# Kernel optimization log

Measured on AMD Instinct MI355X. Metric: run time of the kernel, lower is better.

Reference implementation:

```python
import jax, jax.numpy as jnp
import numpy as np

B, CIN, C, H, W = 4, 256, 128, 64, 64
LN_EPS = 1e-5


def _conv1x1(x, Wk, bk):
    # x: [B, Cin, H, W], Wk: [Cout, Cin] -> [B, Cout, H, W]
    return jnp.einsum('bchw,oc->bohw', x, Wk) + bk[None, :, None, None]


def setup_inputs() -> dict:
    key = jax.random.key(0)
    ks = jax.random.split(key, 11)
    s_in = 1.0 / np.sqrt(CIN)
    s_c = 1.0 / np.sqrt(C)
    return {
        'x': jax.random.normal(ks[0], (B, CIN, H, W), jnp.float32),
        'Wg': jax.random.normal(ks[1], (C, CIN), jnp.float32) * s_in,
        'bg': jax.random.normal(ks[2], (C,), jnp.float32) * s_in,
        'Wt': jax.random.normal(ks[3], (C, CIN), jnp.float32) * s_in,
        'bt': jax.random.normal(ks[4], (C,), jnp.float32) * s_in,
        'Wp': jax.random.normal(ks[5], (C, CIN), jnp.float32) * s_in,
        'bp': jax.random.normal(ks[6], (C,), jnp.float32) * s_in,
        'Wz': jax.random.normal(ks[7], (CIN, C), jnp.float32) * s_c,
        'bz': jax.random.normal(ks[8], (CIN,), jnp.float32) * s_c,
        'gamma': jax.random.normal(ks[9], (CIN, H, W), jnp.float32),
        'beta': jax.random.normal(ks[10], (CIN,), jnp.float32).reshape(CIN, 1, 1) * jnp.ones((CIN, H, W), jnp.float32),
    }


def reference(x, Wg, bg, Wt, bt, Wp, bp, Wz, bz, gamma, beta):
    b, cin, h, w = x.shape
    n = h * w
    # 1x1 conv projections -> flatten spatial
    g = _conv1x1(x, Wg, bg).reshape(b, C, n).transpose(0, 2, 1)      # [B, N, C]
    theta = _conv1x1(x, Wt, bt).reshape(b, C, n).transpose(0, 2, 1)  # [B, N, C]
    phi = _conv1x1(x, Wp, bp).reshape(b, C, n)                        # [B, C, N]
    # embedded-gaussian attention: no scaling, softmax over keys
    f = jnp.einsum('bnc,bcm->bnm', theta, phi)                        # [B, N, N]
    attn = jax.nn.softmax(f, axis=-1)
    y = jnp.einsum('bnm,bmc->bnc', attn, g)                           # [B, N, C]
    y = y.transpose(0, 2, 1).reshape(b, C, h, w)                      # [B, C, H, W]
    # output projection + LayerNorm over [Cin, H, W]
    z = _conv1x1(y, Wz, bz)                                           # [B, Cin, H, W]
    mean = jnp.mean(z, axis=(1, 2, 3), keepdims=True)
    var = jnp.var(z, axis=(1, 2, 3), keepdims=True)
    ln = (z - mean) * jax.lax.rsqrt(var + LN_EPS) * gamma[None] + beta[None]
    return ln + x
```

## Files before the change

kernel.cpp:

```cpp
#include <hip/hip_runtime.h>
#include <hip/hip_bf16.h>


#define BB   4
#define CINC 256
#define CCH  128
#define NS   4096
#define LN_EPS 1e-5f

typedef unsigned short ushort_t;
typedef unsigned int   uint_t;
typedef __bf16 bf16x8 __attribute__((ext_vector_type(8)));
typedef float  f32x4  __attribute__((ext_vector_type(4)));
typedef float  f32x16 __attribute__((ext_vector_type(16)));

typedef const __attribute__((address_space(1))) void* gas_ptr;
typedef __attribute__((address_space(3))) void*       las_ptr;

__device__ __forceinline__ void gload16(const ushort_t* g, ushort_t* l) {
    __builtin_amdgcn_global_load_lds((gas_ptr)g, (las_ptr)l, 16, 0, 0);
}

__device__ __forceinline__ float4 ld4(const float* p) { return *reinterpret_cast<const float4*>(p); }
__device__ __forceinline__ void   st4(float* p, float4 v) { *reinterpret_cast<float4*>(p) = v; }

__device__ __forceinline__ ushort_t f2bf(float f) {
    __hip_bfloat16 h = __float2bfloat16(f);
    return *reinterpret_cast<ushort_t*>(&h);
}
__device__ __forceinline__ float bf2f(ushort_t u) {
    __hip_bfloat16 h = *reinterpret_cast<__hip_bfloat16*>(&u);
    return __bfloat162float(h);
}
__device__ __forceinline__ uint_t pk2(float a, float b) {
    return (uint_t)f2bf(a) | ((uint_t)f2bf(b) << 16);
}

__device__ __forceinline__ float dot4(float4 a, float4 b) {
    return a.x * b.x + a.y * b.y + a.z * b.z + a.w * b.w;
}

__global__ __launch_bounds__(256) void split_kernel(
    const float* __restrict__ x,
    ushort_t* __restrict__ xTh, ushort_t* __restrict__ xTl)
{
    __shared__ float T[64 * 68];

    const int tid = threadIdx.x;
    const int n0  = blockIdx.x * 64;
    const int k0  = blockIdx.y * 64;
    const int b   = blockIdx.z;

#pragma unroll
    for (int u = 0; u < 4; ++u) {
        int fi = u * 256 + tid;
        int k  = fi >> 4;
        int c4 = fi & 15;
        float4 v = ld4(&x[(size_t)(b * CINC + k0 + k) * NS + n0 + c4 * 4]);
        T[(c4 * 4 + 0) * 68 + k] = v.x;
        T[(c4 * 4 + 1) * 68 + k] = v.y;
        T[(c4 * 4 + 2) * 68 + k] = v.z;
        T[(c4 * 4 + 3) * 68 + k] = v.w;
    }
    __syncthreads();

#pragma unroll
    for (int u = 0; u < 2; ++u) {
        int fi = u * 256 + tid;
        int n  = fi >> 3;
        int j  = fi & 7;
        float4 a0 = ld4(&T[n * 68 + j * 8]);
        float4 a1 = ld4(&T[n * 68 + j * 8 + 4]);
        float v[8] = {a0.x, a0.y, a0.z, a0.w, a1.x, a1.y, a1.z, a1.w};
        uint_t hw[4], lw[4];
#pragma unroll
        for (int jj = 0; jj < 4; ++jj) {
            ushort_t h0 = f2bf(v[2 * jj]);
            ushort_t h1 = f2bf(v[2 * jj + 1]);
            ushort_t e0 = f2bf(v[2 * jj] - bf2f(h0));
            ushort_t e1 = f2bf(v[2 * jj + 1] - bf2f(h1));
            hw[jj] = (uint_t)h0 | ((uint_t)h1 << 16);
            lw[jj] = (uint_t)e0 | ((uint_t)e1 << 16);
        }
        size_t base = (size_t)(b * NS + n0 + n) * CINC + k0 + ((j ^ (n & 7)) * 8);
        *reinterpret_cast<uint4*>(&xTh[base]) = make_uint4(hw[0], hw[1], hw[2], hw[3]);
        *reinterpret_cast<uint4*>(&xTl[base]) = make_uint4(lw[0], lw[1], lw[2], lw[3]);
    }
}

__global__ __launch_bounds__(256) void wsplit_kernel(
    const float* __restrict__ Wt, const float* __restrict__ Wp,
    const float* __restrict__ Wg,
    ushort_t* __restrict__ Whs, ushort_t* __restrict__ Wls)
{
    int task = blockIdx.x * 256 + threadIdx.x;
    if (task >= 384 * 32) return;
    int o = task >> 5;
    int j = task & 31;
    int mid = o >> 7;
    int r   = o & 127;
    const float* Wsel = (mid == 0) ? Wt : (mid == 1) ? Wp : Wg;
    float4 a0 = ld4(&Wsel[(size_t)r * CINC + j * 8]);
    float4 a1 = ld4(&Wsel[(size_t)r * CINC + j * 8 + 4]);
    float v[8] = {a0.x, a0.y, a0.z, a0.w, a1.x, a1.y, a1.z, a1.w};
    uint_t hw[4], lw[4];
#pragma unroll
    for (int jj = 0; jj < 4; ++jj) {
        ushort_t h0 = f2bf(v[2 * jj]);
        ushort_t h1 = f2bf(v[2 * jj + 1]);
        ushort_t e0 = f2bf(v[2 * jj] - bf2f(h0));
        ushort_t e1 = f2bf(v[2 * jj + 1] - bf2f(h1));
        hw[jj] = (uint_t)h0 | ((uint_t)h1 << 16);
        lw[jj] = (uint_t)e0 | ((uint_t)e1 << 16);
    }
    int kb = j >> 3, jj8 = j & 7;
    size_t base = (size_t)o * CINC + kb * 64 + ((jj8 ^ (o & 7)) * 8);
    *reinterpret_cast<uint4*>(&Whs[base]) = make_uint4(hw[0], hw[1], hw[2], hw[3]);
    *reinterpret_cast<uint4*>(&Wls[base]) = make_uint4(lw[0], lw[1], lw[2], lw[3]);
}

__global__ __launch_bounds__(256) void proj_mfma_kernel(
    const ushort_t* __restrict__ xTh, const ushort_t* __restrict__ xTl,
    const ushort_t* __restrict__ Whs, const ushort_t* __restrict__ Wls,
    const float* __restrict__ bt, const float* __restrict__ bp,
    const float* __restrict__ bg,
    ushort_t* __restrict__ Qhi, ushort_t* __restrict__ Qlo,
    ushort_t* __restrict__ KhiS, ushort_t* __restrict__ KloS,
    ushort_t* __restrict__ VtS)
{
    __shared__ __align__(16) char smem[65536];
    ushort_t* Wh_l = (ushort_t*)smem;
    ushort_t* Wl_l = (ushort_t*)(smem + 16384);
    ushort_t* Xh_l = (ushort_t*)(smem + 32768);
    ushort_t* Xl_l = (ushort_t*)(smem + 49152);
    float*    T    = (float*)smem;

    const int tid  = threadIdx.x;
    const int w    = tid >> 6;
    const int lane = tid & 63;
    const int l31  = lane & 31;
    const int h    = lane >> 5;
    const int n0   = blockIdx.x * 128;
    const int og   = blockIdx.y;
    const int b    = blockIdx.z;

    const float* bsel = (og == 0) ? bt : (og == 1) ? bp : bg;

    f32x16 acc[4];
#pragma unroll
    for (int ng = 0; ng < 4; ++ng)
#pragma unroll
        for (int r = 0; r < 16; ++r) acc[ng][r] = 0.f;

    const int ol   = w * 32 + l31;
    const int swzq = l31 & 7;

    for (int kb = 0; kb < 4; ++kb) {
        if (kb > 0) __syncthreads();
#pragma unroll
        for (int p = 0; p < 4; ++p) {
            int e  = p * 2048 + tid * 8;
            int rr = e >> 6;
            int kk = e & 63;
            gload16(Whs + (size_t)(og * 128 + rr) * CINC + kb * 64 + kk, Wh_l + e);
            gload16(Wls + (size_t)(og * 128 + rr) * CINC + kb * 64 + kk, Wl_l + e);
            gload16(xTh + (size_t)(b * NS + n0 + rr) * CINC + kb * 64 + kk, Xh_l + e);
            gload16(xTl + (size_t)(b * NS + n0 + rr) * CINC + kb * 64 + kk, Xl_l + e);
        }
        __syncthreads();

        __builtin_amdgcn_s_setprio(1);
#pragma unroll
        for (int k16 = 0; k16 < 4; ++k16) {
            int c8  = k16 * 2 + h;
            int swz = c8 ^ swzq;
            bf16x8 ah = *reinterpret_cast<const bf16x8*>(&Wh_l[ol * 64 + swz * 8]);
            bf16x8 al = *reinterpret_cast<const bf16x8*>(&Wl_l[ol * 64 + swz * 8]);
#pragma unroll
            for (int ng = 0; ng < 4; ++ng) {
                int nl = ng * 32 + l31;
                bf16x8 xh = *reinterpret_cast<const bf16x8*>(&Xh_l[nl * 64 + swz * 8]);
                bf16x8 xl = *reinterpret_cast<const bf16x8*>(&Xl_l[nl * 64 + swz * 8]);
                acc[ng] = __builtin_amdgcn_mfma_f32_32x32x16_bf16(ah, xh, acc[ng], 0, 0, 0);
                acc[ng] = __builtin_amdgcn_mfma_f32_32x32x16_bf16(ah, xl, acc[ng], 0, 0, 0);
                acc[ng] = __builtin_amdgcn_mfma_f32_32x32x16_bf16(al, xh, acc[ng], 0, 0, 0);
            }
        }
        __builtin_amdgcn_s_setprio(0);
    }

    float bv[16];
#pragma unroll
    for (int r = 0; r < 16; ++r)
        bv[r] = bsel[w * 32 + (r & 3) + 8 * (r >> 2) + 4 * h];

    __syncthreads();

    if (og < 2) {
        ushort_t* H = (og == 0) ? Qhi : KhiS;
        ushort_t* L = (og == 0) ? Qlo : KloS;
#pragma unroll
        for (int pass = 0; pass < 2; ++pass) {
#pragma unroll
            for (int ngh = 0; ngh < 2; ++ngh) {
                int ng = pass * 2 + ngh;
                int nl = ngh * 32 + l31;
#pragma unroll
                for (int r = 0; r < 16; ++r) {
                    int o_in = w * 32 + (r & 3) + 8 * (r >> 2) + 4 * h;
                    T[nl * 132 + o_in] = acc[ng][r] + bv[r];
                }
            }
            __syncthreads();
#pragma unroll
            for (int u = 0; u < 4; ++u) {
                int fi = u * 256 + tid;
                int n  = fi >> 4;
                int j  = fi & 15;
                float4 a0 = ld4(&T[n * 132 + j * 8]);
                float4 a1 = ld4(&T[n * 132 + j * 8 + 4]);
                float v[8] = {a0.x, a0.y, a0.z, a0.w, a1.x, a1.y, a1.z, a1.w};
                uint_t hw[4], lw[4];
#pragma unroll
                for (int jj = 0; jj < 4; ++jj) {
                    ushort_t h0 = f2bf(v[2 * jj]);
                    ushort_t h1 = f2bf(v[2 * jj + 1]);
                    ushort_t e0 = f2bf(v[2 * jj] - bf2f(h0));
                    ushort_t e1 = f2bf(v[2 * jj + 1] - bf2f(h1));
                    hw[jj] = (uint_t)h0 | ((uint_t)h1 << 16);
                    lw[jj] = (uint_t)e0 | ((uint_t)e1 << 16);
                }
                int n_glob = n0 + pass * 64 + n;
                int idx = (og == 1) ? ((j & 8) | ((j & 7) ^ (n & 7))) : j;
                size_t base = (size_t)(b * NS + n_glob) * CCH + idx * 8;
                *reinterpret_cast<uint4*>(&H[base]) = make_uint4(hw[0], hw[1], hw[2], hw[3]);
                *reinterpret_cast<uint4*>(&L[base]) = make_uint4(lw[0], lw[1], lw[2], lw[3]);
            }
            __syncthreads();
        }
    } else {
#pragma unroll
        for (int pass = 0; pass < 2; ++pass) {
            if ((w >> 1) == pass) {
#pragma unroll
                for (int ng = 0; ng < 4; ++ng) {
                    int nl = ng * 32 + l31;
#pragma unroll
                    for (int r = 0; r < 16; ++r) {
                        int c_loc = (w & 1) * 32 + (r & 3) + 8 * (r >> 2) + 4 * h;
                        T[c_loc * 132 + nl] = acc[ng][r] + bv[r];
                    }
                }
            }
            __syncthreads();
#pragma unroll
            for (int u = 0; u < 4; ++u) {
                int fi = u * 256 + tid;
                int c_loc = fi >> 4;
                int nj    = fi & 15;
                float4 a0 = ld4(&T[c_loc * 132 + nj * 8]);
                float4 a1 = ld4(&T[c_loc * 132 + nj * 8 + 4]);
                int c = pass * 64 + c_loc;
                uint4 wv;
                wv.x = pk2(a0.x, a0.y);
                wv.y = pk2(a0.z, a0.w);
                wv.z = pk2(a1.x, a1.y);
                wv.w = pk2(a1.z, a1.w);
                size_t base = (size_t)(b * CCH + c) * NS + n0 + (nj >> 3) * 64
                            + (((nj & 7) ^ (c & 7)) * 8);
                *reinterpret_cast<uint4*>(&VtS[base]) = wv;
            }
            __syncthreads();
        }
    }
}

__global__ __launch_bounds__(512, 2) void attn_kernel(
    const ushort_t* __restrict__ Qhi, const ushort_t* __restrict__ Qlo,
    const ushort_t* __restrict__ KhiS, const ushort_t* __restrict__ KloS,
    const ushort_t* __restrict__ VtS, float* __restrict__ Yp,
    float* __restrict__ ML, int NT)
{
    __shared__ __align__(16) char smem[98304];

    const int tid  = threadIdx.x;
    const int w    = tid >> 6;
    const int lane = tid & 63;
    const int l31  = lane & 31;
    const int h    = lane >> 5;
    const int n0   = blockIdx.x * 256;
    const int sp   = blockIdx.y;
    const int b    = blockIdx.z;

    bf16x8 qh[8], ql[8];
    {
        const ushort_t* qrh = Qhi + (size_t)(b * NS + n0 + w * 32 + l31) * CCH;
        const ushort_t* qrl = Qlo + (size_t)(b * NS + n0 + w * 32 + l31) * CCH;
#pragma unroll
        for (int cst = 0; cst < 8; ++cst) {
            qh[cst] = *reinterpret_cast<const bf16x8*>(qrh + cst * 16 + h * 8);
            ql[cst] = *reinterpret_cast<const bf16x8*>(qrl + cst * 16 + h * 8);
        }
    }

    f32x16 yacc[4];
#pragma unroll
    for (int cb = 0; cb < 4; ++cb)
#pragma unroll
        for (int r = 0; r < 16; ++r) yacc[cb][r] = 0.f;
    float m_run = -1e30f, l_run = 0.f;

    const ushort_t* Khg = KhiS + (size_t)b * NS * CCH;
    const ushort_t* Klg = KloS + (size_t)b * NS * CCH;
    const ushort_t* Vtg = VtS + (size_t)b * CCH * NS;

    const int ktbase = sp * NT;

    auto gload_tile = [&](int ktg, int bi) {
        ushort_t* kh = (ushort_t*)(smem + bi * 16384);
        ushort_t* kl = (ushort_t*)(smem + 32768 + bi * 16384);
        ushort_t* vb = (ushort_t*)(smem + 65536 + bi * 16384);
        const size_t koff = (size_t)ktg * 8192;
        const int m0 = ktg * 64;
#pragma unroll
        for (int i = 0; i < 2; ++i) {
            int off = i * 4096 + tid * 8;
            gload16(Khg + koff + off, kh + off);
            gload16(Klg + koff + off, kl + off);
            int cr = off >> 6;
            int cw = off & 63;
            gload16(Vtg + (size_t)cr * NS + m0 + cw, vb + off);
        }
    };

    gload_tile(ktbase, 0);
    __syncthreads();

    const int swzq = l31 & 7;

    for (int kt = 0; kt < NT; ++kt) {
        const int cur = kt & 1;
        const bool more = (kt + 1 < NT);
        if (more) gload_tile(ktbase + kt + 1, cur ^ 1);

        const ushort_t* Kh = (const ushort_t*)(smem + cur * 16384);
        const ushort_t* Kl = (const ushort_t*)(smem + 32768 + cur * 16384);
        const ushort_t* Vl = (const ushort_t*)(smem + 65536 + cur * 16384);

        f32x16 sacc[2];
#pragma unroll
        for (int k2 = 0; k2 < 2; ++k2)
#pragma unroll
            for (int r = 0; r < 16; ++r) sacc[k2][r] = 0.f;

        __builtin_amdgcn_s_setprio(1);
#pragma unroll
        for (int cst = 0; cst < 8; ++cst) {
            int cc  = cst * 2 + h;
            int swz = (cc & 8) | ((cc & 7) ^ swzq);
#pragma unroll
            for (int k2 = 0; k2 < 2; ++k2) {
                int addr = (k2 * 32 + l31) * 128 + swz * 8;
                bf16x8 ah = *reinterpret_cast<const bf16x8*>(&Kh[addr]);
                bf16x8 al = *reinterpret_cast<const bf16x8*>(&Kl[addr]);
                sacc[k2] = __builtin_amdgcn_mfma_f32_32x32x16_bf16(ah, qh[cst], sacc[k2], 0, 0, 0);
                sacc[k2] = __builtin_amdgcn_mfma_f32_32x32x16_bf16(al, qh[cst], sacc[k2], 0, 0, 0);
                sacc[k2] = __builtin_amdgcn_mfma_f32_32x32x16_bf16(ah, ql[cst], sacc[k2], 0, 0, 0);
            }
        }
        __builtin_amdgcn_s_setprio(0);

        float mx = sacc[0][0];
#pragma unroll
        for (int r = 1; r < 16; ++r) mx = fmaxf(mx, sacc[0][r]);
#pragma unroll
        for (int r = 0; r < 16; ++r) mx = fmaxf(mx, sacc[1][r]);
        mx = fmaxf(mx, __shfl_xor(mx, 32));

        const bool defer = __all(mx - m_run <= 8.0f);
        float mref, alpha;
        if (defer) { mref = m_run; alpha = 1.0f; }
        else       { mref = fmaxf(m_run, mx); alpha = __expf(m_run - mref); }

        bf16x8 pb[4];
        float psum = 0.f;
#pragma unroll
        for (int k2 = 0; k2 < 2; ++k2) {
            float pe[16];
#pragma unroll
            for (int r = 0; r < 16; ++r) {
                pe[r] = __expf(sacc[k2][r] - mref);
                psum += pe[r];
            }
#pragma unroll
            for (int a = 0; a < 2; ++a) {
                uint_t w0 = pk2(pe[8 * a + 0], pe[8 * a + 1]);
                uint_t w1 = pk2(pe[8 * a + 2], pe[8 * a + 3]);
                uint_t w2 = pk2(pe[8 * a + 4], pe[8 * a + 5]);
                uint_t w3 = pk2(pe[8 * a + 6], pe[8 * a + 7]);
                uint_t s0 = (uint_t)__shfl_xor((int)w0, 32);
                uint_t s1 = (uint_t)__shfl_xor((int)w1, 32);
                uint_t s2 = (uint_t)__shfl_xor((int)w2, 32);
                uint_t s3 = (uint_t)__shfl_xor((int)w3, 32);
                uint_t u0 = h ? s2 : w0;
                uint_t u1 = h ? s3 : w1;
                uint_t u2 = h ? w2 : s0;
                uint_t u3 = h ? w3 : s1;
                uint4 packed = make_uint4(u0, u1, u2, u3);
                pb[k2 * 2 + a] = *reinterpret_cast<bf16x8*>(&packed);
            }
        }
        psum += __shfl_xor(psum, 32);

        if (defer) {
            l_run += psum;
        } else {
            l_run = l_run * alpha + psum;
            m_run = mref;
#pragma unroll
            for (int cb = 0; cb < 4; ++cb)
#pragma unroll
                for (int r = 0; r < 16; ++r) yacc[cb][r] *= alpha;
        }

        __builtin_amdgcn_s_setprio(1);
#pragma unroll
        for (int cb = 0; cb < 4; ++cb) {
            int crow = (cb * 32 + l31) * 64;
#pragma unroll
            for (int ks = 0; ks < 4; ++ks) {
                int kc = ks * 2 + h;
                bf16x8 av = *reinterpret_cast<const bf16x8*>(&Vl[crow + (kc ^ swzq) * 8]);
                yacc[cb] = __builtin_amdgcn_mfma_f32_32x32x16_bf16(av, pb[ks], yacc[cb], 0, 0, 0);
            }
        }
        __builtin_amdgcn_s_setprio(0);

        __syncthreads();
    }

    float* stage = (float*)smem;
    float* Ybase = Yp + ((size_t)(sp * BB + b) * NS + n0) * CCH;
#pragma unroll
    for (int pass = 0; pass < 4; ++pass) {
        if ((w >> 1) == pass) {
            int qrow = (w & 1) * 32 + l31;
#pragma unroll
            for (int cb = 0; cb < 4; ++cb)
#pragma unroll
                for (int r = 0; r < 16; ++r) {
                    int c = cb * 32 + (r & 3) + 8 * (r >> 2) + 4 * h;
                    stage[qrow * 132 + c] = yacc[cb][r];
                }
        }
        __syncthreads();
#pragma unroll
        for (int u = 0; u < 4; ++u) {
            int idx = u * 512 + tid;
            int row = idx >> 5;
            int c4  = idx & 31;
            st4(&Ybase[(size_t)(pass * 64 + row) * CCH + c4 * 4],
                ld4(&stage[row * 132 + c4 * 4]));
        }
        __syncthreads();
    }
    if (h == 0) {
        size_t mi = ((size_t)(sp * BB + b) * NS + n0 + w * 32 + l31) * 2;
        ML[mi + 0] = m_run;
        ML[mi + 1] = l_run;
    }
}

__global__ __launch_bounds__(256) void merge_kernel(
    const float* __restrict__ Yp, const float* __restrict__ ML,
    float* __restrict__ Ym, int nsplit)
{
    const int total4 = BB * NS * CCH / 4;
    for (int i4 = blockIdx.x * 256 + threadIdx.x; i4 < total4;
         i4 += gridDim.x * 256) {
        int b = i4 >> 17;
        int r = i4 & ((1 << 17) - 1);
        int n = r >> 5;

        float ms[4], ls[4];
        float m = -1e30f;
#pragma unroll
        for (int s = 0; s < 4; ++s) {
            if (s < nsplit) {
                size_t mi = ((size_t)(s * BB + b) * NS + n) * 2;
                ms[s] = ML[mi + 0];
                ls[s] = ML[mi + 1];
                m = fmaxf(m, ms[s]);
            }
        }
        float den = 0.f;
        float wt[4];
#pragma unroll
        for (int s = 0; s < 4; ++s) {
            if (s < nsplit) {
                wt[s] = __expf(ms[s] - m);
                den += ls[s] * wt[s];
            }
        }
        float inv = 1.0f / den;

        float4 acc = make_float4(0.f, 0.f, 0.f, 0.f);
#pragma unroll
        for (int s = 0; s < 4; ++s) {
            if (s < nsplit) {
                float a = wt[s] * inv;
                float4 y = ld4(&Yp[(size_t)(s * BB + b) * NS * CCH + (size_t)r * 4]);
                acc.x += a * y.x;
                acc.y += a * y.y;
                acc.z += a * y.z;
                acc.w += a * y.w;
            }
        }
        st4(&Ym[(size_t)b * NS * CCH + (size_t)r * 4], acc);
    }
}

__global__ __launch_bounds__(256) void zgemm_kernel(
    const float* __restrict__ Ym, const float* __restrict__ Wz,
    const float* __restrict__ bz, float* __restrict__ Z,
    float* __restrict__ partials)
{
    __shared__ float Ws2[64 * 128];
    __shared__ float Ys2[64 * 128];
    __shared__ float red[8];

    const int tid = threadIdx.x;
    const int b   = blockIdx.z;
    const int ot  = blockIdx.y;
    const int n0  = blockIdx.x * 64;
    const int o0  = ot * 64;

#pragma unroll
    for (int u = 0; u < 8; ++u) {
        int fi = tid + 256 * u;
        int row = fi >> 5;
        int kc  = fi & 31;
        st4(&Ws2[row * 128 + (kc ^ (row & 7)) * 4],
            ld4(&Wz[(size_t)(o0 + row) * CCH + kc * 4]));
        st4(&Ys2[row * 128 + (kc ^ (row & 7)) * 4],
            ld4(&Ym[((size_t)b * NS + n0 + row) * CCH + kc * 4]));
    }
    __syncthreads();

    const int q  = tid & 15;
    const int tj = tid >> 4;

    float4 acc[4];
#pragma unroll
    for (int a = 0; a < 4; ++a) acc[a] = make_float4(0.f, 0.f, 0.f, 0.f);
#pragma unroll 4
    for (int g = 0; g < 32; ++g) {
        float4 yv[4], wv[4];
#pragma unroll
        for (int a = 0; a < 4; ++a) {
            int r = q + 16 * a;
            yv[a] = ld4(&Ys2[r * 128 + (g ^ (r & 7)) * 4]);
        }
#pragma unroll
        for (int jj = 0; jj < 4; ++jj) {
            int cj = 4 * tj + jj;
            wv[jj] = ld4(&Ws2[cj * 128 + (g ^ (cj & 7)) * 4]);
        }
#pragma unroll
        for (int a = 0; a < 4; ++a) {
            acc[a].x += dot4(yv[a], wv[0]);
            acc[a].y += dot4(yv[a], wv[1]);
            acc[a].z += dot4(yv[a], wv[2]);
            acc[a].w += dot4(yv[a], wv[3]);
        }
    }

    float4 bz4 = ld4(&bz[o0 + 4 * tj]);
    float s = 0.f, s2 = 0.f;
#pragma unroll
    for (int a = 0; a < 4; ++a) {
        int n = n0 + q + 16 * a;
        float v0 = acc[a].x + bz4.x;
        float v1 = acc[a].y + bz4.y;
        float v2 = acc[a].z + bz4.z;
        float v3 = acc[a].w + bz4.w;
        Z[(size_t)(b * CINC + o0 + 4 * tj + 0) * NS + n] = v0;
        Z[(size_t)(b * CINC + o0 + 4 * tj + 1) * NS + n] = v1;
        Z[(size_t)(b * CINC + o0 + 4 * tj + 2) * NS + n] = v2;
        Z[(size_t)(b * CINC + o0 + 4 * tj + 3) * NS + n] = v3;
        s  += v0 + v1 + v2 + v3;
        s2 += v0 * v0 + v1 * v1 + v2 * v2 + v3 * v3;
    }
#pragma unroll
    for (int off = 1; off < 64; off <<= 1) {
        s  += __shfl_xor(s, off);
        s2 += __shfl_xor(s2, off);
    }
    if ((tid & 63) == 0) { red[(tid >> 6) * 2] = s; red[(tid >> 6) * 2 + 1] = s2; }
    __syncthreads();
    if (tid == 0) {
        float ts  = red[0] + red[2] + red[4] + red[6];
        float ts2 = red[1] + red[3] + red[5] + red[7];
        int pidx = b * 256 + ot * 64 + blockIdx.x;
        partials[pidx * 2 + 0] = ts;
        partials[pidx * 2 + 1] = ts2;
    }
}

__global__ void ln_stats_kernel(const float* __restrict__ partials,
                                float* __restrict__ stats)
{
    const int b = blockIdx.x;
    const int t = threadIdx.x;
    float s = 0.f, s2 = 0.f;
#pragma unroll
    for (int u = 0; u < 4; ++u) {
        const float* pp = &partials[(size_t)(b * 256 + t + 64 * u) * 2];
        s  += pp[0];
        s2 += pp[1];
    }
#pragma unroll
    for (int off = 1; off < 64; off <<= 1) {
        s  += __shfl_xor(s, off);
        s2 += __shfl_xor(s2, off);
    }
    if (t == 0) {
        const float M = 1048576.f;
        float mean = s / M;
        float var  = s2 / M - mean * mean;
        stats[b * 2 + 0] = mean;
        stats[b * 2 + 1] = rsqrtf(var + LN_EPS);
    }
}

__global__ __launch_bounds__(256) void final_kernel(
    const float* __restrict__ Z, const float* __restrict__ x,
    const float* __restrict__ gamma, const float* __restrict__ beta,
    const float* __restrict__ stats, float* __restrict__ out)
{
    const int total4 = BB * CINC * NS / 4;
    for (int i4 = blockIdx.x * 256 + threadIdx.x; i4 < total4;
         i4 += gridDim.x * 256) {
        int b  = i4 >> 18;
        int r4 = i4 & ((1 << 18) - 1);
        float mean = stats[b * 2 + 0];
        float rstd = stats[b * 2 + 1];
        float4 zv = ld4(&Z[(size_t)i4 * 4]);
        float4 xv = ld4(&x[(size_t)i4 * 4]);
        float4 gv = ld4(&gamma[(size_t)r4 * 4]);
        float4 bv = ld4(&beta[(size_t)r4 * 4]);
        float4 o;
        o.x = (zv.x - mean) * rstd * gv.x + bv.x + xv.x;
        o.y = (zv.y - mean) * rstd * gv.y + bv.y + xv.y;
        o.z = (zv.z - mean) * rstd * gv.z + bv.z + xv.z;
        o.w = (zv.w - mean) * rstd * gv.w + bv.w + xv.w;
        st4(&out[(size_t)i4 * 4], o);
    }
}

extern "C" void kernel_launch(void* const* d_in, const int* in_sizes, int n_in,
                              void* d_out, int out_size, void* d_ws, size_t ws_size,
                              hipStream_t stream)
{
    const float* x     = (const float*)d_in[0];
    const float* Wg    = (const float*)d_in[1];
    const float* bg    = (const float*)d_in[2];
    const float* Wt    = (const float*)d_in[3];
    const float* bt    = (const float*)d_in[4];
    const float* Wp    = (const float*)d_in[5];
    const float* bp    = (const float*)d_in[6];
    const float* Wz    = (const float*)d_in[7];
    const float* bz    = (const float*)d_in[8];
    const float* gamma = (const float*)d_in[9];
    const float* beta  = (const float*)d_in[10];
    float* out = (float*)d_out;

    const size_t SZH = (size_t)BB * NS * CCH * sizeof(ushort_t);
    const size_t need4 = 5 * SZH
                       + (size_t)4 * BB * NS * CCH * sizeof(float)
                       + (size_t)4 * BB * NS * 2 * sizeof(float)
                       + (size_t)BB * 256 * 2 * sizeof(float) + 256;
    const int nsplit = (ws_size >= need4) ? 4 : 2;
    const int NT = (NS / 64) / nsplit;

    char* p = (char*)d_ws;
    ushort_t* Qhi  = (ushort_t*)p; p += SZH;
    ushort_t* Qlo  = (ushort_t*)p; p += SZH;
    ushort_t* KhiS = (ushort_t*)p; p += SZH;
    ushort_t* KloS = (ushort_t*)p; p += SZH;
    ushort_t* VtS  = (ushort_t*)p; p += SZH;
    float* Yp = (float*)p; p += (size_t)nsplit * BB * NS * CCH * sizeof(float);
    float* ML = (float*)p; p += (size_t)nsplit * BB * NS * 2 * sizeof(float);
    float* partials = (float*)p; p += BB * 256 * 2 * sizeof(float);
    float* stats    = (float*)p;
    float* Ym = (float*)Qhi;
    float* Z  = (float*)Yp;

    ushort_t* xTh = (ushort_t*)Yp;
    ushort_t* xTl = xTh + (size_t)BB * NS * CINC;
    ushort_t* Whs = (ushort_t*)((char*)Yp + 2 * (size_t)BB * NS * CINC * 2);
    ushort_t* Wls = Whs + (size_t)384 * CINC;

    split_kernel<<<dim3(NS / 64, CINC / 64, BB), 256, 0, stream>>>(x, xTh, xTl);
    wsplit_kernel<<<dim3(48), 256, 0, stream>>>(Wt, Wp, Wg, Whs, Wls);
    proj_mfma_kernel<<<dim3(NS / 128, 3, BB), 256, 0, stream>>>(
        xTh, xTl, Whs, Wls, bt, bp, bg, Qhi, Qlo, KhiS, KloS, VtS);
    attn_kernel<<<dim3(NS / 256, nsplit, BB), 512, 0, stream>>>(
        Qhi, Qlo, KhiS, KloS, VtS, Yp, ML, NT);
    merge_kernel<<<dim3(2048), 256, 0, stream>>>(Yp, ML, Ym, nsplit);
    zgemm_kernel<<<dim3(64, 4, BB), 256, 0, stream>>>(Ym, Wz, bz, Z, partials);
    ln_stats_kernel<<<dim3(BB), 64, 0, stream>>>(partials, stats);
    final_kernel<<<dim3(2048), 256, 0, stream>>>(Z, x, gamma, beta, stats, out);
}
```

Measured before the change: 148.2 us.

## Move output projection to split-bf16 MFMA and shrink attention blocks

The output 1x1 projection GEMM moves from a scalar fp32 LDS kernel to a 3-pass split-bf16 MFMA kernel. The merge kernel now writes hi/lo bf16 swizzled Y, and a new kernel splits Wz the same way. The attention kernel drops from 512 to 256 threads per block (128 queries), loads V single-buffered with an extra barrier, and uses less LDS so more blocks fit per CU. This trades some fp32 accuracy for MFMA throughput, and the single-buffered V load may leave memory latency exposed.

```diff
diff --git a/kernel.cpp b/kernel.cpp
--- a/kernel.cpp
+++ b/kernel.cpp
@@ -36,8 +36,16 @@
     return (uint_t)f2bf(a) | ((uint_t)f2bf(b) << 16);
 }
 
-__device__ __forceinline__ float dot4(float4 a, float4 b) {
-    return a.x * b.x + a.y * b.y + a.z * b.z + a.w * b.w;
+__device__ __forceinline__ void split8(const float* v, uint_t* hw, uint_t* lw) {
+#pragma unroll
+    for (int jj = 0; jj < 4; ++jj) {
+        ushort_t h0 = f2bf(v[2 * jj]);
+        ushort_t h1 = f2bf(v[2 * jj + 1]);
+        ushort_t e0 = f2bf(v[2 * jj] - bf2f(h0));
+        ushort_t e1 = f2bf(v[2 * jj + 1] - bf2f(h1));
+        hw[jj] = (uint_t)h0 | ((uint_t)h1 << 16);
+        lw[jj] = (uint_t)e0 | ((uint_t)e1 << 16);
+    }
 }
 
 __global__ __launch_bounds__(256) void split_kernel(
@@ -73,15 +81,7 @@
         float4 a1 = ld4(&T[n * 68 + j * 8 + 4]);
         float v[8] = {a0.x, a0.y, a0.z, a0.w, a1.x, a1.y, a1.z, a1.w};
         uint_t hw[4], lw[4];
-#pragma unroll
-        for (int jj = 0; jj < 4; ++jj) {
-            ushort_t h0 = f2bf(v[2 * jj]);
-            ushort_t h1 = f2bf(v[2 * jj + 1]);
-            ushort_t e0 = f2bf(v[2 * jj] - bf2f(h0));
-            ushort_t e1 = f2bf(v[2 * jj + 1] - bf2f(h1));
-            hw[jj] = (uint_t)h0 | ((uint_t)h1 << 16);
-            lw[jj] = (uint_t)e0 | ((uint_t)e1 << 16);
-        }
+        split8(v, hw, lw);
         size_t base = (size_t)(b * NS + n0 + n) * CINC + k0 + ((j ^ (n & 7)) * 8);
         *reinterpret_cast<uint4*>(&xTh[base]) = make_uint4(hw[0], hw[1], hw[2], hw[3]);
         *reinterpret_cast<uint4*>(&xTl[base]) = make_uint4(lw[0], lw[1], lw[2], lw[3]);
@@ -104,19 +104,29 @@
     float4 a1 = ld4(&Wsel[(size_t)r * CINC + j * 8 + 4]);
     float v[8] = {a0.x, a0.y, a0.z, a0.w, a1.x, a1.y, a1.z, a1.w};
     uint_t hw[4], lw[4];
-#pragma unroll
-    for (int jj = 0; jj < 4; ++jj) {
-        ushort_t h0 = f2bf(v[2 * jj]);
-        ushort_t h1 = f2bf(v[2 * jj + 1]);
-        ushort_t e0 = f2bf(v[2 * jj] - bf2f(h0));
-        ushort_t e1 = f2bf(v[2 * jj + 1] - bf2f(h1));
-        hw[jj] = (uint_t)h0 | ((uint_t)h1 << 16);
-        lw[jj] = (uint_t)e0 | ((uint_t)e1 << 16);
-    }
+    split8(v, hw, lw);
     int kb = j >> 3, jj8 = j & 7;
     size_t base = (size_t)o * CINC + kb * 64 + ((jj8 ^ (o & 7)) * 8);
     *reinterpret_cast<uint4*>(&Whs[base]) = make_uint4(hw[0], hw[1], hw[2], hw[3]);
     *reinterpret_cast<uint4*>(&Wls[base]) = make_uint4(lw[0], lw[1], lw[2], lw[3]);
+}
+
+__global__ __launch_bounds__(256) void wsplitz_kernel(
+    const float* __restrict__ Wz,
+    ushort_t* __restrict__ Wzh, ushort_t* __restrict__ Wzl)
+{
+    int task = blockIdx.x * 256 + threadIdx.x;
+    if (task >= 256 * 16) return;
+    int o = task >> 4;
+    int j = task & 15;
+    float4 a0 = ld4(&Wz[(size_t)o * CCH + j * 8]);
+    float4 a1 = ld4(&Wz[(size_t)o * CCH + j * 8 + 4]);
+    float v[8] = {a0.x, a0.y, a0.z, a0.w, a1.x, a1.y, a1.z, a1.w};
+    uint_t hw[4], lw[4];
+    split8(v, hw, lw);
+    size_t base = (size_t)o * CCH + (j >> 3) * 64 + (((j & 7) ^ (o & 7)) * 8);
+    *reinterpret_cast<uint4*>(&Wzh[base]) = make_uint4(hw[0], hw[1], hw[2], hw[3]);
+    *reinterpret_cast<uint4*>(&Wzl[base]) = make_uint4(lw[0], lw[1], lw[2], lw[3]);
 }
 
 __global__ __launch_bounds__(256) void proj_mfma_kernel(
@@ -221,15 +231,7 @@
                 float4 a1 = ld4(&T[n * 132 + j * 8 + 4]);
                 float v[8] = {a0.x, a0.y, a0.z, a0.w, a1.x, a1.y, a1.z, a1.w};
                 uint_t hw[4], lw[4];
-#pragma unroll
-                for (int jj = 0; jj < 4; ++jj) {
-                    ushort_t h0 = f2bf(v[2 * jj]);
-                    ushort_t h1 = f2bf(v[2 * jj + 1]);
-                    ushort_t e0 = f2bf(v[2 * jj] - bf2f(h0));
-                    ushort_t e1 = f2bf(v[2 * jj + 1] - bf2f(h1));
-                    hw[jj] = (uint_t)h0 | ((uint_t)h1 << 16);
-                    lw[jj] = (uint_t)e0 | ((uint_t)e1 << 16);
-                }
+                split8(v, hw, lw);
                 int n_glob = n0 + pass * 64 + n;
                 int idx = (og == 1) ? ((j & 8) | ((j & 7) ^ (n & 7))) : j;
                 size_t base = (size_t)(b * NS + n_glob) * CCH + idx * 8;
@@ -275,20 +277,20 @@
     }
 }
 
-__global__ __launch_bounds__(512, 2) void attn_kernel(
+__global__ __launch_bounds__(256, 2) void attn_kernel(
     const ushort_t* __restrict__ Qhi, const ushort_t* __restrict__ Qlo,
     const ushort_t* __restrict__ KhiS, const ushort_t* __restrict__ KloS,
     const ushort_t* __restrict__ VtS, float* __restrict__ Yp,
     float* __restrict__ ML, int NT)
 {
-    __shared__ __align__(16) char smem[98304];
+    __shared__ __align__(16) char smem[81920];
 
     const int tid  = threadIdx.x;
     const int w    = tid >> 6;
     const int lane = tid & 63;
     const int l31  = lane & 31;
     const int h    = lane >> 5;
-    const int n0   = blockIdx.x * 256;
+    const int n0   = blockIdx.x * 128;
     const int sp   = blockIdx.y;
     const int b    = blockIdx.z;
 
@@ -316,24 +318,30 @@
 
     const int ktbase = sp * NT;
 
-    auto gload_tile = [&](int ktg, int bi) {
+    auto gload_k = [&](int ktg, int bi) {
         ushort_t* kh = (ushort_t*)(smem + bi * 16384);
         ushort_t* kl = (ushort_t*)(smem + 32768 + bi * 16384);
-        ushort_t* vb = (ushort_t*)(smem + 65536 + bi * 16384);
         const size_t koff = (size_t)ktg * 8192;
-        const int m0 = ktg * 64;
-#pragma unroll
-        for (int i = 0; i < 2; ++i) {
-            int off = i * 4096 + tid * 8;
+#pragma unroll
+        for (int i = 0; i < 4; ++i) {
+            int off = i * 2048 + tid * 8;
             gload16(Khg + koff + off, kh + off);
             gload16(Klg + koff + off, kl + off);
+        }
+    };
+    auto gload_v = [&](int ktg) {
+        ushort_t* vb = (ushort_t*)(smem + 65536);
+        const int m0 = ktg * 64;
+#pragma unroll
+        for (int i = 0; i < 4; ++i) {
+            int off = i * 2048 + tid * 8;
             int cr = off >> 6;
             int cw = off & 63;
             gload16(Vtg + (size_t)cr * NS + m0 + cw, vb + off);
         }
     };
 
-    gload_tile(ktbase, 0);
+    gload_k(ktbase, 0);
     __syncthreads();
 
     const int swzq = l31 & 7;
@@ -341,11 +349,12 @@
     for (int kt = 0; kt < NT; ++kt) {
         const int cur = kt & 1;
         const bool more = (kt + 1 < NT);
-        if (more) gload_tile(ktbase + kt + 1, cur ^ 1);
+
+        gload_v(ktbase + kt);
+        if (more) gload_k(ktbase + kt + 1, cur ^ 1);
 
         const ushort_t* Kh = (const ushort_t*)(smem + cur * 16384);
         const ushort_t* Kl = (const ushort_t*)(smem + 32768 + cur * 16384);
-        const ushort_t* Vl = (const ushort_t*)(smem + 65536 + cur * 16384);
 
         f32x16 sacc[2];
 #pragma unroll
@@ -412,6 +421,8 @@
         }
         psum += __shfl_xor(psum, 32);
 
+        __syncthreads();
+
         if (defer) {
             l_run += psum;
         } else {
@@ -423,6 +434,7 @@
                 for (int r = 0; r < 16; ++r) yacc[cb][r] *= alpha;
         }
 
+        const ushort_t* Vl = (const ushort_t*)(smem + 65536);
         __builtin_amdgcn_s_setprio(1);
 #pragma unroll
         for (int cb = 0; cb < 4; ++cb) {
@@ -442,7 +454,7 @@
     float* stage = (float*)smem;
     float* Ybase = Yp + ((size_t)(sp * BB + b) * NS + n0) * CCH;
 #pragma unroll
-    for (int pass = 0; pass < 4; ++pass) {
+    for (int pass = 0; pass < 2; ++pass) {
         if ((w >> 1) == pass) {
             int qrow = (w & 1) * 32 + l31;
 #pragma unroll
@@ -455,8 +467,8 @@
         }
         __syncthreads();
 #pragma unroll
-        for (int u = 0; u < 4; ++u) {
-            int idx = u * 512 + tid;
+        for (int u = 0; u < 8; ++u) {
+            int idx = u * 256 + tid;
             int row = idx >> 5;
             int c4  = idx & 31;
             st4(&Ybase[(size_t)(pass * 64 + row) * CCH + c4 * 4],
@@ -473,14 +485,15 @@
 
 __global__ __launch_bounds__(256) void merge_kernel(
     const float* __restrict__ Yp, const float* __restrict__ ML,
-    float* __restrict__ Ym, int nsplit)
-{
-    const int total4 = BB * NS * CCH / 4;
-    for (int i4 = blockIdx.x * 256 + threadIdx.x; i4 < total4;
-         i4 += gridDim.x * 256) {
-        int b = i4 >> 17;
-        int r = i4 & ((1 << 17) - 1);
-        int n = r >> 5;
+    ushort_t* __restrict__ Ymh, ushort_t* __restrict__ Yml, int nsplit)
+{
+    const int total = BB * NS * (CCH / 8);
+    for (int t = blockIdx.x * 256 + threadIdx.x; t < total;
+         t += gridDim.x * 256) {
+        int b = t >> 16;
+        int r = t & 65535;
+        int n = r >> 4;
+        int j = r & 15;
 
         float ms[4], ls[4];
         float m = -1e30f;
@@ -504,104 +517,119 @@
         }
         float inv = 1.0f / den;
 
-        float4 acc = make_float4(0.f, 0.f, 0.f, 0.f);
+        float acc[8] = {0.f, 0.f, 0.f, 0.f, 0.f, 0.f, 0.f, 0.f};
 #pragma unroll
         for (int s = 0; s < 4; ++s) {
             if (s < nsplit) {
                 float a = wt[s] * inv;
-                float4 y = ld4(&Yp[(size_t)(s * BB + b) * NS * CCH + (size_t)r * 4]);
-                acc.x += a * y.x;
-                acc.y += a * y.y;
-                acc.z += a * y.z;
-                acc.w += a * y.w;
-            }
-        }
-        st4(&Ym[(size_t)b * NS * CCH + (size_t)r * 4], acc);
+                const float* yr = &Yp[((size_t)(s * BB + b) * NS + n) * CCH + j * 8];
+                float4 y0 = ld4(yr);
+                float4 y1 = ld4(yr + 4);
+                acc[0] += a * y0.x; acc[1] += a * y0.y;
+                acc[2] += a * y0.z; acc[3] += a * y0.w;
+                acc[4] += a * y1.x; acc[5] += a * y1.y;
+                acc[6] += a * y1.z; acc[7] += a * y1.w;
+            }
+        }
+        uint_t hw[4], lw[4];
+        split8(acc, hw, lw);
+        size_t base = (size_t)(b * NS + n) * CCH + (j >> 3) * 64
+                    + (((j & 7) ^ (n & 7)) * 8);
+        *reinterpret_cast<uint4*>(&Ymh[base]) = make_uint4(hw[0], hw[1], hw[2], hw[3]);
+        *reinterpret_cast<uint4*>(&Yml[base]) = make_uint4(lw[0], lw[1], lw[2], lw[3]);
     }
 }
 
 __global__ __launch_bounds__(256) void zgemm_kernel(
-    const float* __restrict__ Ym, const float* __restrict__ Wz,
+    const ushort_t* __restrict__ Ymh, const ushort_t* __restrict__ Yml,
+    const ushort_t* __restrict__ Wzh, const ushort_t* __restrict__ Wzl,
     const float* __restrict__ bz, float* __restrict__ Z,
     float* __restrict__ partials)
 {
-    __shared__ float Ws2[64 * 128];
-    __shared__ float Ys2[64 * 128];
+    __shared__ __align__(16) char smem[65536];
+    ushort_t* Wh_l = (ushort_t*)smem;
+    ushort_t* Wl_l = (ushort_t*)(smem + 16384);
+    ushort_t* Yh_l = (ushort_t*)(smem + 32768);
+    ushort_t* Yl_l = (ushort_t*)(smem + 49152);
     __shared__ float red[8];
 
-    const int tid = threadIdx.x;
-    const int b   = blockIdx.z;
-    const int ot  = blockIdx.y;
-    const int n0  = blockIdx.x * 64;
-    const int o0  = ot * 64;
-
-#pragma unroll
-    for (int u = 0; u < 8; ++u) {
-        int fi = tid + 256 * u;
-        int row = fi >> 5;
-        int kc  = fi & 31;
-        st4(&Ws2[row * 128 + (kc ^ (row & 7)) * 4],
-            ld4(&Wz[(size_t)(o0 + row) * CCH + kc * 4]));
-        st4(&Ys2[row * 128 + (kc ^ (row & 7)) * 4],
-            ld4(&Ym[((size_t)b * NS + n0 + row) * CCH + kc * 4]));
-    }
-    __syncthreads();
-
-    const int q  = tid & 15;
-    const int tj = tid >> 4;
-
-    float4 acc[4];
-#pragma unroll
-    for (int a = 0; a < 4; ++a) acc[a] = make_float4(0.f, 0.f, 0.f, 0.f);
-#pragma unroll 4
-    for (int g = 0; g < 32; ++g) {
-        float4 yv[4], wv[4];
-#pragma unroll
-        for (int a = 0; a < 4; ++a) {
-            int r = q + 16 * a;
-            yv[a] = ld4(&Ys2[r * 128 + (g ^ (r & 7)) * 4]);
-        }
-#pragma unroll
-        for (int jj = 0; jj < 4; ++jj) {
-            int cj = 4 * tj + jj;
-            wv[jj] = ld4(&Ws2[cj * 128 + (g ^ (cj & 7)) * 4]);
-        }
-#pragma unroll
-        for (int a = 0; a < 4; ++a) {
-            acc[a].x += dot4(yv[a], wv[0]);
-            acc[a].y += dot4(yv[a], wv[1]);
-            acc[a].z += dot4(yv[a], wv[2]);
-            acc[a].w += dot4(yv[a], wv[3]);
-        }
-    }
-
-    float4 bz4 = ld4(&bz[o0 + 4 * tj]);
+    const int tid  = threadIdx.x;
+    const int w    = tid >> 6;
+    const int lane = tid & 63;
+    const int l31  = lane & 31;
+    const int h    = lane >> 5;
+    const int n0   = blockIdx.x * 128;
+    const int o0   = blockIdx.y * 128;
+    const int b    = blockIdx.z;
+
+    f32x16 acc[4];
+#pragma unroll
+    for (int ng = 0; ng < 4; ++ng)
+#pragma unroll
+        for (int r = 0; r < 16; ++r) acc[ng][r] = 0.f;
+
+    const int ol   = w * 32 + l31;
+    const int swzq = l31 & 7;
+
+    for (int kb = 0; kb < 2; ++kb) {
+        if (kb > 0) __syncthreads();
+#pragma unroll
+        for (int p = 0; p < 4; ++p) {
+            int e  = p * 2048 + tid * 8;
+            int rr = e >> 6;
+            int kk = e & 63;
+            gload16(Wzh + (size_t)(o0 + rr) * CCH + kb * 64 + kk, Wh_l + e);
+            gload16(Wzl + (size_t)(o0 + rr) * CCH + kb * 64 + kk, Wl_l + e);
+            gload16(Ymh + (size_t)(b * NS + n0 + rr) * CCH + kb * 64 + kk, Yh_l + e);
+            gload16(Yml + (size_t)(b * NS + n0 + rr) * CCH + kb * 64 + kk, Yl_l + e);
+        }
+        __syncthreads();
+
+        __builtin_amdgcn_s_setprio(1);
+#pragma unroll
+        for (int k16 = 0; k16 < 4; ++k16) {
+            int c8  = k16 * 2 + h;
+            int swz = c8 ^ swzq;
+            bf16x8 ah = *reinterpret_cast<const bf16x8*>(&Wh_l[ol * 64 + swz * 8]);
+            bf16x8 al = *reinterpret_cast<const bf16x8*>(&Wl_l[ol * 64 + swz * 8]);
+#pragma unroll
+            for (int ng = 0; ng < 4; ++ng) {
+                int nl = ng * 32 + l31;
+                bf16x8 yh = *reinterpret_cast<const bf16x8*>(&Yh_l[nl * 64 + swz * 8]);
+                bf16x8 yl = *reinterpret_cast<const bf16x8*>(&Yl_l[nl * 64 + swz * 8]);
+                acc[ng] = __builtin_amdgcn_mfma_f32_32x32x16_bf16(ah, yh, acc[ng], 0, 0, 0);
+                acc[ng] = __builtin_amdgcn_mfma_f32_32x32x16_bf16(ah, yl, acc[ng], 0, 0, 0);
+                acc[ng] = __builtin_amdgcn_mfma_f32_32x32x16_bf16(al, yh, acc[ng], 0, 0, 0);
+            }
+        }
+        __builtin_amdgcn_s_setprio(0);
+    }
+
     float s = 0.f, s2 = 0.f;
 #pragma unroll
-    for (int a = 0; a < 4; ++a) {
-        int n = n0 + q + 16 * a;
-        float v0 = acc[a].x + bz4.x;
-        float v1 = acc[a].y + bz4.y;
-        float v2 = acc[a].z + bz4.z;
-        float v3 = acc[a].w + bz4.w;
-        Z[(size_t)(b * CINC + o0 + 4 * tj + 0) * NS + n] = v0;
-        Z[(size_t)(b * CINC + o0 + 4 * tj + 1) * NS + n] = v1;
-        Z[(size_t)(b * CINC + o0 + 4 * tj + 2) * NS + n] = v2;
-        Z[(size_t)(b * CINC + o0 + 4 * tj + 3) * NS + n] = v3;
-        s  += v0 + v1 + v2 + v3;
-        s2 += v0 * v0 + v1 * v1 + v2 * v2 + v3 * v3;
+    for (int r = 0; r < 16; ++r) {
+        int o = o0 + w * 32 + (r & 3) + 8 * (r >> 2) + 4 * h;
+        float bias = bz[o];
+        float* zrow = &Z[(size_t)(b * CINC + o) * NS + n0 + l31];
+#pragma unroll
+        for (int ng = 0; ng < 4; ++ng) {
+            float v = acc[ng][r] + bias;
+            zrow[ng * 32] = v;
+            s  += v;
+            s2 += v * v;
+        }
     }
 #pragma unroll
     for (int off = 1; off < 64; off <<= 1) {
         s  += __shfl_xor(s, off);
         s2 += __shfl_xor(s2, off);
     }
-    if ((tid & 63) == 0) { red[(tid >> 6) * 2] = s; red[(tid >> 6) * 2 + 1] = s2; }
+    if (lane == 0) { red[w * 2] = s; red[w * 2 + 1] = s2; }
     __syncthreads();
     if (tid == 0) {
         float ts  = red[0] + red[2] + red[4] + red[6];
         float ts2 = red[1] + red[3] + red[5] + red[7];
-        int pidx = b * 256 + ot * 64 + blockIdx.x;
+        int pidx = (b * 2 + blockIdx.y) * 32 + blockIdx.x;
         partials[pidx * 2 + 0] = ts;
         partials[pidx * 2 + 1] = ts2;
     }
@@ -612,13 +640,8 @@
 {
     const int b = blockIdx.x;
     const int t = threadIdx.x;
-    float s = 0.f, s2 = 0.f;
-#pragma unroll
-    for (int u = 0; u < 4; ++u) {
-        const float* pp = &partials[(size_t)(b * 256 + t + 64 * u) * 2];
-        s  += pp[0];
-        s2 += pp[1];
-    }
+    float s  = partials[(size_t)(b * 64 + t) * 2 + 0];
+    float s2 = partials[(size_t)(b * 64 + t) * 2 + 1];
 #pragma unroll
     for (int off = 1; off < 64; off <<= 1) {
         s  += __shfl_xor(s, off);
@@ -679,7 +702,7 @@
     const size_t need4 = 5 * SZH
                        + (size_t)4 * BB * NS * CCH * sizeof(float)
                        + (size_t)4 * BB * NS * 2 * sizeof(float)
-                       + (size_t)BB * 256 * 2 * sizeof(float) + 256;
+                       + (size_t)BB * 64 * 2 * sizeof(float) + 256;
     const int nsplit = (ws_size >= need4) ? 4 : 2;
     const int NT = (NS / 64) / nsplit;
 
@@ -691,10 +714,14 @@
     ushort_t* VtS  = (ushort_t*)p; p += SZH;
     float* Yp = (float*)p; p += (size_t)nsplit * BB * NS * CCH * sizeof(float);
     float* ML = (float*)p; p += (size_t)nsplit * BB * NS * 2 * sizeof(float);
-    float* partials = (float*)p; p += BB * 256 * 2 * sizeof(float);
+    float* partials = (float*)p; p += BB * 64 * 2 * sizeof(float);
     float* stats    = (float*)p;
-    float* Ym = (float*)Qhi;
-    float* Z  = (float*)Yp;
+
+    ushort_t* Ymh = (ushort_t*)Qhi;
+    ushort_t* Yml = (ushort_t*)Qlo;
+    ushort_t* Wzh = (ushort_t*)KhiS;
+    ushort_t* Wzl = (ushort_t*)KloS;
+    float*    Z   = (float*)Yp;
 
     ushort_t* xTh = (ushort_t*)Yp;
     ushort_t* xTl = xTh + (size_t)BB * NS * CINC;
@@ -705,10 +732,12 @@
     wsplit_kernel<<<dim3(48), 256, 0, stream>>>(Wt, Wp, Wg, Whs, Wls);
     proj_mfma_kernel<<<dim3(NS / 128, 3, BB), 256, 0, stream>>>(
         xTh, xTl, Whs, Wls, bt, bp, bg, Qhi, Qlo, KhiS, KloS, VtS);
-    attn_kernel<<<dim3(NS / 256, nsplit, BB), 512, 0, stream>>>(
+    attn_kernel<<<dim3(NS / 128, nsplit, BB), 256, 0, stream>>>(
         Qhi, Qlo, KhiS, KloS, VtS, Yp, ML, NT);
-    merge_kernel<<<dim3(2048), 256, 0, stream>>>(Yp, ML, Ym, nsplit);
-    zgemm_kernel<<<dim3(64, 4, BB), 256, 0, stream>>>(Ym, Wz, bz, Z, partials);
+    wsplitz_kernel<<<dim3(16), 256, 0, stream>>>(Wz, Wzh, Wzl);
+    merge_kernel<<<dim3(1024), 256, 0, stream>>>(Yp, ML, Ymh, Yml, nsplit);
+    zgemm_kernel<<<dim3(NS / 128, 2, BB), 256, 0, stream>>>(
+        Ymh, Yml, Wzh, Wzl, bz, Z, partials);
     ln_stats_kernel<<<dim3(BB), 64, 0, stream>>>(partials, stats);
     final_kernel<<<dim3(2048), 256, 0, stream>>>(Z, x, gamma, beta, stats, out);
 }
```

Measured after the change: 133.9 us. 9.7% less time.
